# Performance work log

Hardware: AMD Instinct MI355X
Metric: run time of the kernel (lower is better)

Reference implementation:

```python
import jax, jax.numpy as jnp
import numpy as np

NUM_PL, NUM_TR, NUM_AR = 50000, 100000, 10000
HID, FEAT, NUM_LAYERS = 64, 128, 2


def setup_inputs() -> dict:
    key = jax.random.key(0)
    ks = jax.random.split(key, 16)
    inp = {
        'track_x': jax.random.normal(ks[0], (NUM_TR, FEAT), dtype=jnp.float32),
        'pl_tr_src': jax.random.randint(ks[1], (2000000,), 0, NUM_PL, dtype=jnp.int32),
        'pl_tr_dst': jax.random.randint(ks[2], (2000000,), 0, NUM_TR, dtype=jnp.int32),
        'tr_ar_src': jax.random.randint(ks[3], (100000,), 0, NUM_TR, dtype=jnp.int32),
        'tr_ar_dst': jax.random.randint(ks[4], (100000,), 0, NUM_AR, dtype=jnp.int32),
        # learned parameters
        'playlist_emb': jax.random.normal(ks[5], (NUM_PL, HID), dtype=jnp.float32),
        'artist_emb': jax.random.normal(ks[6], (NUM_AR, HID), dtype=jnp.float32),
        'track_W': jax.random.normal(ks[7], (HID, FEAT), dtype=jnp.float32) / np.sqrt(FEAT),
        'track_b': jnp.zeros((HID,), dtype=jnp.float32),
        'type_emb': jax.random.normal(ks[8], (3, HID), dtype=jnp.float32),
        # SAGEConv params per layer: lin_l (neighbor, with bias), lin_r (root, no bias)
        'conv_Wl': jax.random.normal(ks[9], (NUM_LAYERS, HID, HID), dtype=jnp.float32) / np.sqrt(HID),
        'conv_bl': jnp.zeros((NUM_LAYERS, HID), dtype=jnp.float32),
        'conv_Wr': jax.random.normal(ks[10], (NUM_LAYERS, HID, HID), dtype=jnp.float32) / np.sqrt(HID),
    }
    return inp


def reference(track_x, pl_tr_src, pl_tr_dst, tr_ar_src, tr_ar_dst,
              playlist_emb, artist_emb, track_W, track_b, type_emb,
              conv_Wl, conv_bl, conv_Wr):
    off_tr = NUM_PL
    off_ar = NUM_PL + NUM_TR
    N = NUM_PL + NUM_TR + NUM_AR

    # node features: [playlist_emb; track_lin(track_x); artist_emb] + type_emb[type]
    x_tr = track_x @ track_W.T + track_b
    x = jnp.concatenate([playlist_emb, x_tr, artist_emb], axis=0)
    type_ids = jnp.concatenate([
        jnp.zeros((NUM_PL,), jnp.int32),
        jnp.ones((NUM_TR,), jnp.int32),
        jnp.full((NUM_AR,), 2, jnp.int32)])
    x = x + type_emb[type_ids]

    # combined edge index: pl->tr, tr->pl, tr->ar, ar->tr (global node ids)
    pl = pl_tr_src
    tr1 = pl_tr_dst + off_tr
    tr2 = tr_ar_src + off_tr
    ar = tr_ar_dst + off_ar
    src = jnp.concatenate([pl, tr1, tr2, ar])
    dst = jnp.concatenate([tr1, pl, ar, tr2])

    # mean-aggregation degrees (clamped to avoid div by 0)
    deg = jax.ops.segment_sum(jnp.ones_like(src, dtype=x.dtype), dst, num_segments=N)
    deg = jnp.maximum(deg, 1.0)[:, None]

    for l in range(NUM_LAYERS):
        agg = jax.ops.segment_sum(x[src], dst, num_segments=N) / deg  # mean over neighbors
        x = jax.nn.relu(agg @ conv_Wl[l].T + conv_bl[l] + x @ conv_Wr[l].T)

    return (x[:off_tr], x[off_tr:off_ar], x[off_ar:])
```

## Files before the change

kernel.cpp:

```cpp
#include <hip/hip_runtime.h>

#define NUM_PL 50000
#define NUM_TR 100000
#define NUM_AR 10000
#define NN     160000
#define HID    64
#define FEAT   128
#define E_PLTR 2000000
#define E_TRAR 100000
#define E_TOT  4200000
#define OFF_TR 50000
#define OFF_AR 150000

#define BIN_CHUNK 4096
#define NBLK_BIN  1026
#define NBUCK     625
#define TABW      626
#define PKD_CAP   (NBLK_BIN * BIN_CHUNK)

#define WSTR 65

#define SCAP 11520

__device__ __forceinline__ float h2f(ushort u) {
  _Float16 h = __builtin_bit_cast(_Float16, u);
  return (float)h;
}
__device__ __forceinline__ ushort f2h(float f) {
  _Float16 h = (_Float16)f;
  return __builtin_bit_cast(ushort, h);
}

__device__ __forceinline__ void fmix_lo(float& a, uint u) {
  asm("v_fma_mix_f32 %0, %1, 1.0, %0 op_sel_hi:[1,0,0]"
      : "+v"(a) : "v"(u));
}
__device__ __forceinline__ void fmix_hi(float& a, uint u) {
  asm("v_fma_mix_f32 %0, %1, 1.0, %0 op_sel:[1,0,0] op_sel_hi:[1,0,0]"
      : "+v"(a) : "v"(u));
}
__device__ __forceinline__ void acc_h4(float4& a, ushort4 u) {
  uint2 w = __builtin_bit_cast(uint2, u);
  fmix_lo(a.x, w.x); fmix_hi(a.y, w.x);
  fmix_lo(a.z, w.y); fmix_hi(a.w, w.y);
}

__device__ __forceinline__ void edge_sd(
    int e, const int* __restrict__ pls, const int* __restrict__ pld,
    const int* __restrict__ tas, const int* __restrict__ tad, int& s, int& d) {
  if (e < E_PLTR)                   { s = pls[e];               d = pld[e] + OFF_TR; }
  else if (e < 2 * E_PLTR)          { int i = e - E_PLTR;
                                      s = pld[i] + OFF_TR;      d = pls[i]; }
  else if (e < 2 * E_PLTR + E_TRAR) { int i = e - 2 * E_PLTR;
                                      s = tas[i] + OFF_TR;      d = tad[i] + OFF_AR; }
  else                              { int i = e - 2 * E_PLTR - E_TRAR;
                                      s = tad[i] + OFF_AR;      d = tas[i] + OFF_TR; }
}

__global__ __launch_bounds__(256) void k_init_emb(
    const float* __restrict__ pl_emb, const float* __restrict__ ar_emb,
    const float* __restrict__ type_emb, float* __restrict__ x,
    ushort* __restrict__ xh) {
  int tid = blockIdx.x * 256 + threadIdx.x;
  int f = tid & (HID - 1);
  if (tid < NUM_PL * HID) {
    float v = pl_emb[tid] + type_emb[f];
    x[tid] = v;
    xh[tid] = f2h(v);
  } else {
    int idx = tid - NUM_PL * HID;
    if (idx < NUM_AR * HID) {
      float v = ar_emb[idx] + type_emb[2 * HID + f];
      x[OFF_AR * HID + idx] = v;
      xh[OFF_AR * HID + idx] = f2h(v);
    }
  }
}

__global__ __launch_bounds__(256) void k_track_lin(
    const float* __restrict__ tx, const float* __restrict__ W,
    const float* __restrict__ b, const float* __restrict__ type_emb,
    float* __restrict__ x, ushort* __restrict__ xh) {
  __shared__ float WS[FEAT * 65];
  __shared__ float bs[HID];
  int t = threadIdx.x;
  for (int idx = t; idx < HID * FEAT; idx += 256) {
    int j = idx >> 7, k = idx & (FEAT - 1);
    WS[k * 65 + j] = W[idx];
  }
  if (t < HID) bs[t] = b[t] + type_emb[HID + t];
  __syncthreads();

  int j  = t & 63;
  int wv = __builtin_amdgcn_readfirstlane(t >> 6);
  int row0 = blockIdx.x * 32 + wv * 8;
  const float* xr = tx + (size_t)row0 * FEAT;

  float acc[8] = {0.f, 0.f, 0.f, 0.f, 0.f, 0.f, 0.f, 0.f};
#pragma unroll 4
  for (int k = 0; k < FEAT; ++k) {
    float w = WS[k * 65 + j];
#pragma unroll
    for (int r = 0; r < 8; ++r)
      acc[r] += xr[r * FEAT + k] * w;
  }
#pragma unroll
  for (int r = 0; r < 8; ++r) {
    float v = acc[r] + bs[j];
    x[(OFF_TR + row0 + r) * HID + j] = v;
    xh[(OFF_TR + row0 + r) * HID + j] = f2h(v);
  }
}

__global__ __launch_bounds__(256) void k_bin(
    const int* __restrict__ pls, const int* __restrict__ pld,
    const int* __restrict__ tas, const int* __restrict__ tad,
    int* __restrict__ pkd, int* __restrict__ tab, int* __restrict__ btot) {
  __shared__ int    pkL[BIN_CHUNK];
  __shared__ ushort bL[BIN_CHUNK];
  __shared__ int hist[TABW];
  __shared__ int offs[TABW];
  __shared__ int scanbuf[256];
  int t = threadIdx.x;
  int blk = blockIdx.x;
  int e0 = blk * BIN_CHUNK;
  int e1 = e0 + BIN_CHUNK; if (e1 > E_TOT) e1 = E_TOT;

  for (int i = t; i < TABW; i += 256) hist[i] = 0;
  __syncthreads();

  for (int e = e0 + t; e < e1; e += 256) {
    int s, d; edge_sd(e, pls, pld, tas, tad, s, d);
    int b = min(max(d >> 8, 0), NBUCK - 1);
    int li = e - e0;
    pkL[li] = ((d & 255) << 18) | s;
    bL[li] = (ushort)b;
    atomicAdd(&hist[b], 1);
  }
  __syncthreads();

  int i0 = 3 * t, i1 = 3 * t + 1, i2 = 3 * t + 2;
  int h0 = (i0 < NBUCK) ? hist[i0] : 0;
  int h1 = (i1 < NBUCK) ? hist[i1] : 0;
  int h2 = (i2 < NBUCK) ? hist[i2] : 0;
  if (i0 < NBUCK && h0) atomicAdd(&btot[i0], h0);
  if (i1 < NBUCK && h1) atomicAdd(&btot[i1], h1);
  if (i2 < NBUCK && h2) atomicAdd(&btot[i2], h2);
  int lsum = h0 + h1 + h2;
  scanbuf[t] = lsum;
  __syncthreads();
  int incl = lsum;
#pragma unroll
  for (int off = 1; off < 256; off <<= 1) {
    int add = (t >= off) ? scanbuf[t - off] : 0;
    __syncthreads();
    incl += add;
    scanbuf[t] = incl;
    __syncthreads();
  }
  int base = incl - lsum;
  if (i0 < TABW) offs[i0] = base;
  if (i1 < TABW) offs[i1] = base + h0;
  if (i2 < TABW) offs[i2] = base + h0 + h1;
  __syncthreads();

  for (int i = t; i < TABW; i += 256) tab[blk * TABW + i] = e0 + offs[i];
  for (int i = t; i < NBUCK; i += 256) hist[i] = offs[i];
  __syncthreads();

  for (int e = e0 + t; e < e1; e += 256) {
    int li = e - e0;
    int b = bL[li];
    int pos = atomicAdd(&hist[b], 1);
    int idx = min(max(e0 + pos, 0), PKD_CAP - 1);
    pkd[idx] = pkL[li];
  }
}

__global__ __launch_bounds__(1024) void k_bscan(int* __restrict__ btot) {
  __shared__ int s[1024];
  int t = threadIdx.x;
  int val = (t < NBUCK) ? btot[t] : 0;
  s[t] = val;
  __syncthreads();
  int incl = val;
#pragma unroll
  for (int off = 1; off < 1024; off <<= 1) {
    int add = (t >= off) ? s[t - off] : 0;
    __syncthreads();
    incl += add;
    s[t] = incl;
    __syncthreads();
  }
  if (t < NBUCK) btot[t] = incl - val;
}

__global__ __launch_bounds__(256) void k_fill3(
    const int* __restrict__ tab, const int* __restrict__ pkd,
    const int* __restrict__ btot, int* __restrict__ rowptr,
    int* __restrict__ col) {
  __shared__ int stage[SCAP];
  __shared__ int cnt[256];
  __shared__ int scanbuf[256];
  __shared__ int validS;
  int t = threadIdx.x;
  int b = blockIdx.x;

  int len = 0;
  for (int blk = t; blk < NBLK_BIN; blk += 256) {
    int s0 = tab[blk * TABW + b];
    int s1 = tab[blk * TABW + b + 1];
    s0 = min(max(s0, 0), PKD_CAP);
    s1 = min(max(s1, s0), PKD_CAP);
    len += s1 - s0;
  }

  cnt[t] = 0;
  if (t == 0) validS = 0x7fffffff;
  scanbuf[t] = len;
  __syncthreads();
  int incl = len;
#pragma unroll
  for (int off = 1; off < 256; off <<= 1) {
    int add = (t >= off) ? scanbuf[t - off] : 0;
    __syncthreads();
    incl += add;
    scanbuf[t] = incl;
    __syncthreads();
  }
  int base = incl - len;
  int totalE = scanbuf[255];
  bool fits = (base + len <= SCAP);
  if (!fits) atomicMin(&validS, base);
  __syncthreads();
  int valid = min(validS, totalE);

  int off = base;
  for (int blk = t; blk < NBLK_BIN; blk += 256) {
    int s0 = tab[blk * TABW + b];
    int s1 = tab[blk * TABW + b + 1];
    s0 = min(max(s0, 0), PKD_CAP);
    s1 = min(max(s1, s0), PKD_CAP);
    for (int i = s0; i < s1; ++i) {
      int pk = pkd[i];
      atomicAdd(&cnt[(pk >> 18) & 255], 1);
      if (fits) stage[off++] = pk;
    }
  }
  __syncthreads();

  int val = cnt[t];
  scanbuf[t] = val;
  __syncthreads();
  incl = val;
#pragma unroll
  for (int off2 = 1; off2 < 256; off2 <<= 1) {
    int add = (t >= off2) ? scanbuf[t - off2] : 0;
    __syncthreads();
    incl += add;
    scanbuf[t] = incl;
    __syncthreads();
  }
  int rp = btot[b] + incl - val;
  rowptr[(b << 8) + t] = rp;
  if (b == NBUCK - 1 && t == 255) rowptr[NN] = E_TOT;
  __syncthreads();
  cnt[t] = rp;
  __syncthreads();

  for (int i = t; i < valid; i += 256) {
    int pk = stage[i];
    int pos = atomicAdd(&cnt[(pk >> 18) & 255], 1);
    pos = min(max(pos, 0), E_TOT - 1);
    col[pos] = pk & 0x3FFFF;
  }
  if (!fits) {
    for (int blk = t; blk < NBLK_BIN; blk += 256) {
      int s0 = tab[blk * TABW + b];
      int s1 = tab[blk * TABW + b + 1];
      s0 = min(max(s0, 0), PKD_CAP);
      s1 = min(max(s1, s0), PKD_CAP);
      for (int i = s0; i < s1; ++i) {
        int pk = pkd[i];
        int pos = atomicAdd(&cnt[(pk >> 18) & 255], 1);
        pos = min(max(pos, 0), E_TOT - 1);
        col[pos] = pk & 0x3FFFF;
      }
    }
  }
}

__global__ __launch_bounds__(1024, 8) void k_gather_update(
    const int* __restrict__ rowptr, const int* __restrict__ col,
    const ushort* __restrict__ xh,
    const float* __restrict__ Wl, const float* __restrict__ bl,
    const float* __restrict__ Wr,
    ushort* __restrict__ xnh, float* __restrict__ xnf) {
  __shared__ float WlS[HID * WSTR];
  __shared__ float WrS[HID * WSTR];
  __shared__ float bs[HID];
  __shared__ __align__(16) float rowS[16][4][2 * HID];
  int t = threadIdx.x;
  for (int idx = t; idx < HID * HID; idx += 1024) {
    int j = idx >> 6, k = idx & 63;
    WlS[k * WSTR + j] = Wl[idx];
    WrS[k * WSTR + j] = Wr[idx];
  }
  if (t < HID) bs[t] = bl[t];
  __syncthreads();

  int lane = t & 63;
  int wv = t >> 6;
  int r = lane >> 4;
  int c = lane & 15;
  const ushort4* xh4 = (const ushort4*)xh;
  int nbase = (blockIdx.x * 16 + wv) * 4;

  for (int it = 0; it < 4; ++it) {
    int n = nbase + it;
    int rp0 = rowptr[n], rp1 = rowptr[n + 1];

    ushort4 ru;
    if (r == 0) ru = xh4[n * 16 + c];

    float4 a0 = {0.f, 0.f, 0.f, 0.f};
    float4 a1 = {0.f, 0.f, 0.f, 0.f};
    float4 a2 = {0.f, 0.f, 0.f, 0.f};
    float4 a3 = {0.f, 0.f, 0.f, 0.f};
    int base = rp0;
    for (; base + 16 <= rp1; base += 16) {
      int s0 = col[base + r];
      int s1 = col[base + 4 + r];
      int s2 = col[base + 8 + r];
      int s3 = col[base + 12 + r];
      ushort4 u0 = xh4[s0 * 16 + c];
      ushort4 u1 = xh4[s1 * 16 + c];
      ushort4 u2 = xh4[s2 * 16 + c];
      ushort4 u3 = xh4[s3 * 16 + c];
      acc_h4(a0, u0);
      acc_h4(a1, u1);
      acc_h4(a2, u2);
      acc_h4(a3, u3);
    }
    if (base + 4 <= rp1) {
      int s0 = col[base + r];
      acc_h4(a0, xh4[s0 * 16 + c]);
      base += 4;
    }
    if (base + 4 <= rp1) {
      int s1 = col[base + r];
      acc_h4(a1, xh4[s1 * 16 + c]);
      base += 4;
    }
    if (base + 4 <= rp1) {
      int s2 = col[base + r];
      acc_h4(a2, xh4[s2 * 16 + c]);
      base += 4;
    }
    if (base + r < rp1) {
      int s3 = col[base + r];
      acc_h4(a3, xh4[s3 * 16 + c]);
    }
    float4 a;
    a.x = (a0.x + a1.x) + (a2.x + a3.x);
    a.y = (a0.y + a1.y) + (a2.y + a3.y);
    a.z = (a0.z + a1.z) + (a2.z + a3.z);
    a.w = (a0.w + a1.w) + (a2.w + a3.w);
    a.x += __shfl_xor(a.x, 16); a.y += __shfl_xor(a.y, 16);
    a.z += __shfl_xor(a.z, 16); a.w += __shfl_xor(a.w, 16);
    a.x += __shfl_xor(a.x, 32); a.y += __shfl_xor(a.y, 32);
    a.z += __shfl_xor(a.z, 32); a.w += __shfl_xor(a.w, 32);

    if (r == 0) {
      float id = 1.0f / (float)max(rp1 - rp0, 1);
      float4 o;
      o.x = a.x * id; o.y = a.y * id; o.z = a.z * id; o.w = a.w * id;
      float4 rootf;
      rootf.x = h2f(ru.x); rootf.y = h2f(ru.y);
      rootf.z = h2f(ru.z); rootf.w = h2f(ru.w);
      ((float4*)&rowS[wv][it][0])[c] = o;
      ((float4*)&rowS[wv][it][0])[16 + c] = rootf;
    }
  }

  asm volatile("s_waitcnt lgkmcnt(0)" ::: "memory");
  __builtin_amdgcn_sched_barrier(0);

  const float4* row0 = (const float4*)&rowS[wv][0][0];
  const float4* row1 = (const float4*)&rowS[wv][1][0];
  const float4* row2 = (const float4*)&rowS[wv][2][0];
  const float4* row3 = (const float4*)&rowS[wv][3][0];
  float acc0 = 0.f, acc1 = 0.f, acc2 = 0.f, acc3 = 0.f;
#pragma unroll 2
  for (int k4 = 0; k4 < 16; ++k4) {
    float4 g0 = row0[k4], t0 = row0[16 + k4];
    float4 g1 = row1[k4], t1 = row1[16 + k4];
    float4 g2 = row2[k4], t2 = row2[16 + k4];
    float4 g3 = row3[k4], t3 = row3[16 + k4];
    int k = k4 * 4;
    float wl0 = WlS[(k + 0) * WSTR + lane], wr0 = WrS[(k + 0) * WSTR + lane];
    float wl1 = WlS[(k + 1) * WSTR + lane], wr1 = WrS[(k + 1) * WSTR + lane];
    float wl2 = WlS[(k + 2) * WSTR + lane], wr2 = WrS[(k + 2) * WSTR + lane];
    float wl3 = WlS[(k + 3) * WSTR + lane], wr3 = WrS[(k + 3) * WSTR + lane];
    acc0 += g0.x * wl0 + g0.y * wl1 + g0.z * wl2 + g0.w * wl3
          + t0.x * wr0 + t0.y * wr1 + t0.z * wr2 + t0.w * wr3;
    acc1 += g1.x * wl0 + g1.y * wl1 + g1.z * wl2 + g1.w * wl3
          + t1.x * wr0 + t1.y * wr1 + t1.z * wr2 + t1.w * wr3;
    acc2 += g2.x * wl0 + g2.y * wl1 + g2.z * wl2 + g2.w * wl3
          + t2.x * wr0 + t2.y * wr1 + t2.z * wr2 + t2.w * wr3;
    acc3 += g3.x * wl0 + g3.y * wl1 + g3.z * wl2 + g3.w * wl3
          + t3.x * wr0 + t3.y * wr1 + t3.z * wr2 + t3.w * wr3;
  }
  float bias = bs[lane];
  float o0 = fmaxf(acc0 + bias, 0.f);
  float o1 = fmaxf(acc1 + bias, 0.f);
  float o2 = fmaxf(acc2 + bias, 0.f);
  float o3 = fmaxf(acc3 + bias, 0.f);
  if (xnf) {
    xnf[(nbase + 0) * HID + lane] = o0;
    xnf[(nbase + 1) * HID + lane] = o1;
    xnf[(nbase + 2) * HID + lane] = o2;
    xnf[(nbase + 3) * HID + lane] = o3;
  } else {
    xnh[(nbase + 0) * HID + lane] = f2h(o0);
    xnh[(nbase + 1) * HID + lane] = f2h(o1);
    xnh[(nbase + 2) * HID + lane] = f2h(o2);
    xnh[(nbase + 3) * HID + lane] = f2h(o3);
  }
}

extern "C" void kernel_launch(void* const* d_in, const int* in_sizes, int n_in,
                              void* d_out, int out_size, void* d_ws, size_t ws_size,
                              hipStream_t stream) {
  const float* track_x  = (const float*)d_in[0];
  const int*   pl_tr_s  = (const int*)d_in[1];
  const int*   pl_tr_d  = (const int*)d_in[2];
  const int*   tr_ar_s  = (const int*)d_in[3];
  const int*   tr_ar_d  = (const int*)d_in[4];
  const float* pl_emb   = (const float*)d_in[5];
  const float* ar_emb   = (const float*)d_in[6];
  const float* track_W  = (const float*)d_in[7];
  const float* track_b  = (const float*)d_in[8];
  const float* type_emb = (const float*)d_in[9];
  const float* conv_Wl  = (const float*)d_in[10];
  const float* conv_bl  = (const float*)d_in[11];
  const float* conv_Wr  = (const float*)d_in[12];

  float* x = (float*)d_out;

  char* w = (char*)d_ws;
  ushort* xh1   = (ushort*)w;
  int*   pkd    = (int*)w;
  int*   tab    = (int*)(w + (size_t)PKD_CAP * 4);
  w += (size_t)NN * HID * 2;
  ushort* xh0   = (ushort*)w; w += (size_t)NN * HID * 2;
  int*   col    = (int*)w;    w += (size_t)E_TOT * 4;
  int*   rowptr = (int*)w;    w += (size_t)(NN + 1) * 4;
  int*   btot   = (int*)w;

  hipMemsetAsync(btot, 0, NBUCK * sizeof(int), stream);

  k_init_emb<<<(NUM_PL + NUM_AR) * HID / 256, 256, 0, stream>>>(
      pl_emb, ar_emb, type_emb, x, xh0);
  k_track_lin<<<NUM_TR / 32, 256, 0, stream>>>(
      track_x, track_W, track_b, type_emb, x, xh0);

  k_bin<<<NBLK_BIN, 256, 0, stream>>>(
      pl_tr_s, pl_tr_d, tr_ar_s, tr_ar_d, pkd, tab, btot);
  k_bscan<<<1, 1024, 0, stream>>>(btot);
  k_fill3<<<NBUCK, 256, 0, stream>>>(tab, pkd, btot, rowptr, col);

  k_gather_update<<<NN / 64, 1024, 0, stream>>>(
      rowptr, col, xh0, conv_Wl, conv_bl, conv_Wr, xh1, nullptr);
  k_gather_update<<<NN / 64, 1024, 0, stream>>>(
      rowptr, col, xh1, conv_Wl + HID * HID, conv_bl + HID,
      conv_Wr + HID * HID, xh0 , x);
}
```

Measured before the change: 615.1 us.

## Use MFMA f16 matrix cores for per-block SAGE linear update

Replaces the per-wave scalar FP32 dot-product loop over shared-memory weights with a block-level 64x64x128 GEMM using MFMA 16x16x16 f16 instructions. Aggregated means and root features are staged as fp16 in shared memory, and the concatenated Wl|Wr weights are stored as fp16. A block-wide barrier is added between the gather phase and the matrix phase. Rounding the aggregated mean to fp16 before the multiply adds precision error, and the shared-memory footprint changes.

```diff
diff --git a/kernel.cpp b/kernel.cpp
--- a/kernel.cpp
+++ b/kernel.cpp
@@ -18,9 +18,11 @@
 #define TABW      626
 #define PKD_CAP   (NBLK_BIN * BIN_CHUNK)
 
-#define WSTR 65
-
 #define SCAP 11520
+#define MSTR 132
+
+typedef _Float16 half4v __attribute__((ext_vector_type(4)));
+typedef float    f32x4  __attribute__((ext_vector_type(4)));
 
 __device__ __forceinline__ float h2f(ushort u) {
   _Float16 h = __builtin_bit_cast(_Float16, u);
@@ -296,15 +298,14 @@
     const float* __restrict__ Wl, const float* __restrict__ bl,
     const float* __restrict__ Wr,
     ushort* __restrict__ xnh, float* __restrict__ xnf) {
-  __shared__ float WlS[HID * WSTR];
-  __shared__ float WrS[HID * WSTR];
+  __shared__ _Float16 WcatS[64 * MSTR];
+  __shared__ _Float16 MS[64 * MSTR];
   __shared__ float bs[HID];
-  __shared__ __align__(16) float rowS[16][4][2 * HID];
   int t = threadIdx.x;
   for (int idx = t; idx < HID * HID; idx += 1024) {
     int j = idx >> 6, k = idx & 63;
-    WlS[k * WSTR + j] = Wl[idx];
-    WrS[k * WSTR + j] = Wr[idx];
+    WcatS[j * MSTR + k]      = (_Float16)Wl[idx];
+    WcatS[j * MSTR + 64 + k] = (_Float16)Wr[idx];
   }
   if (t < HID) bs[t] = bl[t];
   __syncthreads();
@@ -314,10 +315,11 @@
   int r = lane >> 4;
   int c = lane & 15;
   const ushort4* xh4 = (const ushort4*)xh;
-  int nbase = (blockIdx.x * 16 + wv) * 4;
+  int Nb = blockIdx.x * 64;
 
   for (int it = 0; it < 4; ++it) {
-    int n = nbase + it;
+    int nloc = wv * 4 + it;
+    int n = Nb + nloc;
     int rp0 = rowptr[n], rp1 = rowptr[n + 1];
 
     ushort4 ru;
@@ -373,59 +375,40 @@
 
     if (r == 0) {
       float id = 1.0f / (float)max(rp1 - rp0, 1);
-      float4 o;
-      o.x = a.x * id; o.y = a.y * id; o.z = a.z * id; o.w = a.w * id;
-      float4 rootf;
-      rootf.x = h2f(ru.x); rootf.y = h2f(ru.y);
-      rootf.z = h2f(ru.z); rootf.w = h2f(ru.w);
-      ((float4*)&rowS[wv][it][0])[c] = o;
-      ((float4*)&rowS[wv][it][0])[16 + c] = rootf;
-    }
-  }
-
-  asm volatile("s_waitcnt lgkmcnt(0)" ::: "memory");
-  __builtin_amdgcn_sched_barrier(0);
-
-  const float4* row0 = (const float4*)&rowS[wv][0][0];
-  const float4* row1 = (const float4*)&rowS[wv][1][0];
-  const float4* row2 = (const float4*)&rowS[wv][2][0];
-  const float4* row3 = (const float4*)&rowS[wv][3][0];
-  float acc0 = 0.f, acc1 = 0.f, acc2 = 0.f, acc3 = 0.f;
-#pragma unroll 2
-  for (int k4 = 0; k4 < 16; ++k4) {
-    float4 g0 = row0[k4], t0 = row0[16 + k4];
-    float4 g1 = row1[k4], t1 = row1[16 + k4];
-    float4 g2 = row2[k4], t2 = row2[16 + k4];
-    float4 g3 = row3[k4], t3 = row3[16 + k4];
-    int k = k4 * 4;
-    float wl0 = WlS[(k + 0) * WSTR + lane], wr0 = WrS[(k + 0) * WSTR + lane];
-    float wl1 = WlS[(k + 1) * WSTR + lane], wr1 = WrS[(k + 1) * WSTR + lane];
-    float wl2 = WlS[(k + 2) * WSTR + lane], wr2 = WrS[(k + 2) * WSTR + lane];
-    float wl3 = WlS[(k + 3) * WSTR + lane], wr3 = WrS[(k + 3) * WSTR + lane];
-    acc0 += g0.x * wl0 + g0.y * wl1 + g0.z * wl2 + g0.w * wl3
-          + t0.x * wr0 + t0.y * wr1 + t0.z * wr2 + t0.w * wr3;
-    acc1 += g1.x * wl0 + g1.y * wl1 + g1.z * wl2 + g1.w * wl3
-          + t1.x * wr0 + t1.y * wr1 + t1.z * wr2 + t1.w * wr3;
-    acc2 += g2.x * wl0 + g2.y * wl1 + g2.z * wl2 + g2.w * wl3
-          + t2.x * wr0 + t2.y * wr1 + t2.z * wr2 + t2.w * wr3;
-    acc3 += g3.x * wl0 + g3.y * wl1 + g3.z * wl2 + g3.w * wl3
-          + t3.x * wr0 + t3.y * wr1 + t3.z * wr2 + t3.w * wr3;
-  }
-  float bias = bs[lane];
-  float o0 = fmaxf(acc0 + bias, 0.f);
-  float o1 = fmaxf(acc1 + bias, 0.f);
-  float o2 = fmaxf(acc2 + bias, 0.f);
-  float o3 = fmaxf(acc3 + bias, 0.f);
+      half4v ah;
+      ah[0] = (_Float16)(a.x * id); ah[1] = (_Float16)(a.y * id);
+      ah[2] = (_Float16)(a.z * id); ah[3] = (_Float16)(a.w * id);
+      *(half4v*)&MS[nloc * MSTR + 4 * c] = ah;
+      *(half4v*)&MS[nloc * MSTR + 64 + 4 * c] =
+          __builtin_bit_cast(half4v, ru);
+    }
+  }
+
+  __syncthreads();
+
+  int mt = wv >> 2, nt = wv & 3;
+  int ml = lane & 15, g = lane >> 4;
+  const _Float16* arow = &MS[(mt * 16 + ml) * MSTR];
+  const _Float16* brow = &WcatS[(nt * 16 + ml) * MSTR];
+  f32x4 acc = {0.f, 0.f, 0.f, 0.f};
+#pragma unroll
+  for (int kt = 0; kt < 8; ++kt) {
+    int kb = kt * 16 + 4 * g;
+    half4v af = *(const half4v*)&arow[kb];
+    half4v bf = *(const half4v*)&brow[kb];
+    acc = __builtin_amdgcn_mfma_f32_16x16x16f16(af, bf, acc, 0, 0, 0);
+  }
+  int j = nt * 16 + ml;
+  float bias = bs[j];
+  int nrow0 = Nb + mt * 16 + 4 * g;
   if (xnf) {
-    xnf[(nbase + 0) * HID + lane] = o0;
-    xnf[(nbase + 1) * HID + lane] = o1;
-    xnf[(nbase + 2) * HID + lane] = o2;
-    xnf[(nbase + 3) * HID + lane] = o3;
+#pragma unroll
+    for (int i = 0; i < 4; ++i)
+      xnf[(nrow0 + i) * HID + j] = fmaxf(acc[i] + bias, 0.f);
   } else {
-    xnh[(nbase + 0) * HID + lane] = f2h(o0);
-    xnh[(nbase + 1) * HID + lane] = f2h(o1);
-    xnh[(nbase + 2) * HID + lane] = f2h(o2);
-    xnh[(nbase + 3) * HID + lane] = f2h(o3);
+#pragma unroll
+    for (int i = 0; i < 4; ++i)
+      xnh[(nrow0 + i) * HID + j] = f2h(fmaxf(acc[i] + bias, 0.f));
   }
 }
 
```

New measurement: 558.6 us. -9.2%, faster.
